# Performance work log

Hardware: AMD Instinct MI355X
Metric: run time of the kernel (lower is better)

Reference implementation:

```python
import jax, jax.numpy as jnp
import numpy as np

LEVELS = 16
BASE_RES = 16.0
MAX_RES = 2048.0
MAX_PARAMS = 2 ** 19
FEAT = 2
LOG_B = np.log(MAX_RES / BASE_RES) / (LEVELS - 1)
PRIMES = np.array([1, 2654435761, 805459861], dtype=np.uint32)


def level_meta():
    # Replays HashEncoder.__init__ offset/size bookkeeping.
    offsets, sizes, ress = [], [], []
    offset = 0
    begin_fast = LEVELS
    for i in range(LEVELS):
        res = int(np.ceil(BASE_RES * np.exp(i * LOG_B) - 1.0) + 1)  # grid_resolution
        full = float(res) ** 3
        aligned = int((full + 7) / 8) * 8  # align_to(full, 8)
        size = int(min(MAX_PARAMS, aligned))
        if full > size and begin_fast == LEVELS:
            begin_fast = i
        offsets.append(offset)
        sizes.append(size)
        ress.append(res)
        offset += size
    return offsets, sizes, ress, begin_fast, offset


OFFSETS, SIZES, RESS, BEGIN_FAST, TOTAL = level_meta()


def setup_inputs():
    key = jax.random.key(0)
    k1, k2 = jax.random.split(key)
    B = 2_000_000
    positions = jax.random.uniform(k1, (B, 3), dtype=jnp.float32)  # xyz in [0,1)
    table = jax.random.uniform(k2, (TOTAL, FEAT), dtype=jnp.float32,
                               minval=-1e-4, maxval=1e-4)
    return {"positions": positions, "table": table}


def _encode(positions, table):
    outs = []
    for level in range(LEVELS):  # fixed small structural loop (16 levels)
        scale = np.float32(BASE_RES * np.exp(level * LOG_B) - 1.0)  # grid_scale
        res = RESS[level]
        pos = positions * scale + 0.5          # [B,3]
        grid_f = jnp.floor(pos)
        frac = pos - grid_f                    # [B,3] trilinear fractions
        grid = grid_f.astype(jnp.uint32)
        acc = jnp.zeros((positions.shape[0], FEAT), dtype=jnp.float32)
        for corner in range(8):                # 8 cube corners (static unroll)
            sel = np.array([(corner >> d) & 1 for d in range(3)], dtype=np.uint32)
            pg = grid + sel                    # [B,3] uint32 corner coords
            w = jnp.prod(jnp.where(sel.astype(bool), frac, 1.0 - frac), axis=-1)  # [B]
            if level < BEGIN_FAST:
                # dense 'under_hash': x + y*res + z*res^2 (uint32 wraparound ok)
                strides = np.array([1, res, res * res], dtype=np.uint32)
                h = jnp.sum(pg * strides, axis=-1, dtype=jnp.uint32)
            else:
                # spatial 'fast_hash': xor of coord*prime with uint32 wraparound
                h = (pg[:, 0] * PRIMES[0]) ^ (pg[:, 1] * PRIMES[1]) ^ (pg[:, 2] * PRIMES[2])
            idx = (h % np.uint32(SIZES[level])).astype(jnp.int32) + OFFSETS[level]
            acc = acc + w[:, None] * table[idx]  # irregular gather [B,FEAT]
        outs.append(acc)
    # matches output_embedding[i, level].view(-1, levels*feat): level-major, feat inner
    return jnp.concatenate(outs, axis=-1)  # [B, LEVELS*FEAT]


def reference(positions, table):
    return _encode(positions, table)
```

## Files before the change

### kernel.cpp

```cpp
#include <hip/hip_runtime.h>
#include <math.h>

#define NLEVELS 16
#define BEGIN_FAST 5
#define P2 2654435761u
#define P3 805459861u
#define FAST_MASK 524287u

constexpr unsigned kRes[NLEVELS] = {16u, 23u, 31u, 43u, 59u, 81u, 112u, 154u, 213u, 295u, 407u, 562u, 777u, 1073u, 1483u, 2048u};
constexpr unsigned kSize[NLEVELS] = {
    4096u, 12168u, 29792u, 79512u, 205384u,
    524288u, 524288u, 524288u, 524288u, 524288u, 524288u,
    524288u, 524288u, 524288u, 524288u, 524288u};
constexpr unsigned kOffset[NLEVELS] = {
    0u,       4096u,    16264u,   46056u,   125568u,  330952u,
    855240u,  1379528u, 1903816u, 2428104u, 2952392u, 3476680u,
    4000968u, 4525256u, 5049544u, 5573832u};

struct Scales {
    float s[NLEVELS];
};

typedef float fvec2 __attribute__((ext_vector_type(2)));
typedef float fvec4 __attribute__((ext_vector_type(4)));
typedef float fvec4a8 __attribute__((ext_vector_type(4), aligned(8)));

__global__ __launch_bounds__(256) void fine_level_kernel(
    const float* __restrict__ positions,
    const float2* __restrict__ tab,
    float2* __restrict__ wsl,
    int B, float s)
{
    int p = blockIdx.x * 256 + threadIdx.x;
    if (p >= B) return;

    const float x = __builtin_nontemporal_load(positions + 3 * p + 0);
    const float y = __builtin_nontemporal_load(positions + 3 * p + 1);
    const float z = __builtin_nontemporal_load(positions + 3 * p + 2);

    const float px = x * s + 0.5f;
    const float py = y * s + 0.5f;
    const float pz = z * s + 0.5f;
    const float flx = floorf(px), fly = floorf(py), flz = floorf(pz);
    const float rx = px - flx, ry = py - fly, rz = pz - flz;
    const unsigned gx = (unsigned)flx;
    const unsigned gy = (unsigned)fly;
    const unsigned gz = (unsigned)flz;
    const float wx0 = 1.0f - rx, wy0 = 1.0f - ry, wz0 = 1.0f - rz;

    const unsigned hy0 = gy * P2, hy1 = hy0 + P2;
    const unsigned hz0 = gz * P3, hz1 = hz0 + P3;

    float ax = 0.0f, ay = 0.0f;
#pragma unroll
    for (int c = 0; c < 8; ++c) {
        const unsigned cx = (unsigned)(c & 1);
        const unsigned cy = (unsigned)((c >> 1) & 1);
        const unsigned cz = (unsigned)((c >> 2) & 1);
        const float w = (cx ? rx : wx0) * (cy ? ry : wy0) * (cz ? rz : wz0);
        const unsigned h = (gx + cx) ^ (cy ? hy1 : hy0) ^ (cz ? hz1 : hz0);
        const float2 t = tab[h & FAST_MASK];
        ax += w * t.x;
        ay += w * t.y;
    }
    fvec2 r = {ax, ay};
    __builtin_nontemporal_store(r, reinterpret_cast<fvec2*>(wsl) + p);
}

__global__ __launch_bounds__(256) void dense_kernel(
    const float* __restrict__ positions,
    const float2* __restrict__ table,
    float2* __restrict__ ws,
    int B, Scales sc)
{
    int p = blockIdx.x * 256 + threadIdx.x;
    if (p >= B) return;

    const float x = __builtin_nontemporal_load(positions + 3 * p + 0);
    const float y = __builtin_nontemporal_load(positions + 3 * p + 1);
    const float z = __builtin_nontemporal_load(positions + 3 * p + 2);

#pragma unroll
    for (int l = 0; l < BEGIN_FAST; ++l) {
        const float s = sc.s[l];
        const float px = x * s + 0.5f;
        const float py = y * s + 0.5f;
        const float pz = z * s + 0.5f;
        const float flx = floorf(px), fly = floorf(py), flz = floorf(pz);
        const float rx = px - flx, ry = py - fly, rz = pz - flz;
        const unsigned gx = (unsigned)flx;
        const unsigned gy = (unsigned)fly;
        const unsigned gz = (unsigned)flz;
        const float wx0 = 1.0f - rx, wy0 = 1.0f - ry, wz0 = 1.0f - rz;

        const float2* tab = table + kOffset[l];
        const unsigned res = kRes[l];

        float ax = 0.0f, ay = 0.0f;
#pragma unroll
        for (int cc = 0; cc < 4; ++cc) {
            const unsigned cy = (unsigned)(cc & 1);
            const unsigned cz = (unsigned)(cc >> 1);
            const float wyz = (cy ? ry : wy0) * (cz ? rz : wz0);
            const unsigned h0 = gx + (gy + cy) * res + (gz + cz) * (res * res);
            const unsigned idx0 = h0 % kSize[l];
            const fvec4 tt = *reinterpret_cast<const fvec4a8*>(tab + idx0);
            float t1x = tt.z, t1y = tt.w;
            if (idx0 == kSize[l] - 1) {
                const float2 tf = tab[0];
                t1x = tf.x; t1y = tf.y;
            }
            ax += wyz * (wx0 * tt.x + rx * t1x);
            ay += wyz * (wx0 * tt.y + rx * t1y);
        }
        fvec2 r = {ax, ay};
        __builtin_nontemporal_store(r, reinterpret_cast<fvec2*>(ws) + (size_t)l * (size_t)B + p);
    }
}

__global__ __launch_bounds__(256) void merge_kernel(
    const float2* __restrict__ ws,
    float* __restrict__ out,
    int B)
{
    int p = blockIdx.x * 256 + threadIdx.x;
    if (p >= B) return;

    float o[2 * NLEVELS];
#pragma unroll
    for (int l = 0; l < NLEVELS; ++l) {
        const fvec2 v = __builtin_nontemporal_load(
            reinterpret_cast<const fvec2*>(ws) + (size_t)l * (size_t)B + p);
        o[2 * l + 0] = v.x;
        o[2 * l + 1] = v.y;
    }
    float* op = out + (size_t)p * (2 * NLEVELS);
#pragma unroll
    for (int i = 0; i < 8; ++i) {
        fvec4 v = {o[4 * i + 0], o[4 * i + 1], o[4 * i + 2], o[4 * i + 3]};
        *(reinterpret_cast<fvec4*>(op) + i) = v;
    }
}

__global__ __launch_bounds__(256) void final_kernel(
    const float* __restrict__ positions,
    const float2* __restrict__ table,
    const float2* __restrict__ ws,
    float* __restrict__ out,
    int B, Scales sc)
{
    int p = blockIdx.x * 256 + threadIdx.x;
    if (p >= B) return;

    const float x = positions[3 * p + 0];
    const float y = positions[3 * p + 1];
    const float z = positions[3 * p + 2];

    float o[2 * NLEVELS];

#pragma unroll
    for (int l = 0; l < BEGIN_FAST; ++l) {
        const float s = sc.s[l];
        const float px = x * s + 0.5f;
        const float py = y * s + 0.5f;
        const float pz = z * s + 0.5f;
        const float flx = floorf(px), fly = floorf(py), flz = floorf(pz);
        const float rx = px - flx, ry = py - fly, rz = pz - flz;
        const unsigned gx = (unsigned)flx;
        const unsigned gy = (unsigned)fly;
        const unsigned gz = (unsigned)flz;
        const float wx0 = 1.0f - rx, wy0 = 1.0f - ry, wz0 = 1.0f - rz;

        float ax = 0.0f, ay = 0.0f;
#pragma unroll
        for (int c = 0; c < 8; ++c) {
            const unsigned cx = (unsigned)(c & 1);
            const unsigned cy = (unsigned)((c >> 1) & 1);
            const unsigned cz = (unsigned)((c >> 2) & 1);
            const float w = (cx ? rx : wx0) * (cy ? ry : wy0) * (cz ? rz : wz0);
            const unsigned h = (gx + cx) + (gy + cy) * kRes[l] + (gz + cz) * (kRes[l] * kRes[l]);
            const float2 t = table[(h % kSize[l]) + kOffset[l]];
            ax += w * t.x;
            ay += w * t.y;
        }
        o[2 * l + 0] = ax;
        o[2 * l + 1] = ay;
    }

#pragma unroll
    for (int l = BEGIN_FAST; l < NLEVELS; ++l) {
        const float2 v = ws[(size_t)(l - BEGIN_FAST) * (size_t)B + p];
        o[2 * l + 0] = v.x;
        o[2 * l + 1] = v.y;
    }

    float* op = out + (size_t)p * (2 * NLEVELS);
#pragma unroll
    for (int i = 0; i < 8; ++i) {
        fvec4 v = {o[4 * i + 0], o[4 * i + 1], o[4 * i + 2], o[4 * i + 3]};
        *(reinterpret_cast<fvec4*>(op) + i) = v;
    }
}

extern "C" void kernel_launch(void* const* d_in, const int* in_sizes, int n_in,
                              void* d_out, int out_size, void* d_ws, size_t ws_size,
                              hipStream_t stream) {
    const float* positions = (const float*)d_in[0];
    const float2* table = (const float2*)d_in[1];
    float* out = (float*)d_out;

    const int B = in_sizes[0] / 3;

    Scales sc;
    const double log_b = log(2048.0 / 16.0) / (NLEVELS - 1);
    for (int l = 0; l < NLEVELS; ++l) {
        sc.s[l] = (float)(16.0 * exp((double)l * log_b) - 1.0);
    }

    const int blocks = (B + 255) / 256;
    const size_t slice_bytes = (size_t)B * sizeof(float2);
    float2* ws = (float2*)d_ws;

    if (ws_size >= (size_t)NLEVELS * slice_bytes) {
        for (int l = BEGIN_FAST; l < NLEVELS; ++l) {
            fine_level_kernel<<<blocks, 256, 0, stream>>>(
                positions, table + kOffset[l],
                ws + (size_t)l * (size_t)B, B, sc.s[l]);
        }
        dense_kernel<<<blocks, 256, 0, stream>>>(positions, table, ws, B, sc);
        merge_kernel<<<blocks, 256, 0, stream>>>(ws, out, B);
    } else {
        for (int l = BEGIN_FAST; l < NLEVELS; ++l) {
            fine_level_kernel<<<blocks, 256, 0, stream>>>(
                positions, table + kOffset[l],
                ws + (size_t)(l - BEGIN_FAST) * (size_t)B, B, sc.s[l]);
        }
        final_kernel<<<blocks, 256, 0, stream>>>(positions, table, ws, out, B, sc);
    }
}
```

Baseline: 828.7 us.

## Store per-level encodings as packed bf16 and pair x-corner gathers in fine levels

Per-level intermediate results are packed as two bf16 values in one 32-bit word instead of float2, halving workspace writes and merge reads. The fine hash-level kernel exploits that even gx makes the two x-neighbour hash indices adjacent, fetching both with one 16-byte load and issuing a second gather only for odd gx. The fallback path becomes a single fused kernel computing all levels. The bf16 rounding reduces output precision and may violate accuracy tolerance.

```diff
diff --git a/kernel.cpp b/kernel.cpp
--- a/kernel.cpp
+++ b/kernel.cpp
@@ -25,10 +25,18 @@
 typedef float fvec4 __attribute__((ext_vector_type(4)));
 typedef float fvec4a8 __attribute__((ext_vector_type(4), aligned(8)));
 
+__device__ __forceinline__ unsigned bfpack(float a, float b) {
+    unsigned ua = __float_as_uint(a);
+    unsigned ub = __float_as_uint(b);
+    ua = (ua + 0x7FFFu + ((ua >> 16) & 1u)) >> 16;
+    ub = (ub + 0x7FFFu + ((ub >> 16) & 1u)) & 0xFFFF0000u;
+    return ua | ub;
+}
+
 __global__ __launch_bounds__(256) void fine_level_kernel(
     const float* __restrict__ positions,
     const float2* __restrict__ tab,
-    float2* __restrict__ wsl,
+    unsigned* __restrict__ wsl,
     int B, float s)
 {
     int p = blockIdx.x * 256 + threadIdx.x;
@@ -50,27 +58,40 @@
 
     const unsigned hy0 = gy * P2, hy1 = hy0 + P2;
     const unsigned hz0 = gz * P3, hz1 = hz0 + P3;
+    const bool odd = (gx & 1u) != 0u;
+    const unsigned gx1 = gx + 1u;
 
     float ax = 0.0f, ay = 0.0f;
 #pragma unroll
-    for (int c = 0; c < 8; ++c) {
-        const unsigned cx = (unsigned)(c & 1);
-        const unsigned cy = (unsigned)((c >> 1) & 1);
-        const unsigned cz = (unsigned)((c >> 2) & 1);
-        const float w = (cx ? rx : wx0) * (cy ? ry : wy0) * (cz ? rz : wz0);
-        const unsigned h = (gx + cx) ^ (cy ? hy1 : hy0) ^ (cz ? hz1 : hz0);
-        const float2 t = tab[h & FAST_MASK];
-        ax += w * t.x;
-        ay += w * t.y;
-    }
-    fvec2 r = {ax, ay};
-    __builtin_nontemporal_store(r, reinterpret_cast<fvec2*>(wsl) + p);
+    for (int cc = 0; cc < 4; ++cc) {
+        const unsigned cy = (unsigned)(cc & 1);
+        const unsigned cz = (unsigned)(cc >> 1);
+        const float wyz = (cy ? ry : wy0) * (cz ? rz : wz0);
+        const unsigned A = (cy ? hy1 : hy0) ^ (cz ? hz1 : hz0);
+        const unsigned i0 = (gx ^ A) & FAST_MASK;
+        const unsigned base = i0 & ~1u;
+        const fvec4 tt = *reinterpret_cast<const fvec4*>(tab + base);
+        const bool lo = (i0 & 1u) == 0u;
+        const float e0x = lo ? tt.x : tt.z;
+        const float e0y = lo ? tt.y : tt.w;
+        float e1x = lo ? tt.z : tt.x;
+        float e1y = lo ? tt.w : tt.y;
+        if (odd) {
+            const unsigned i1 = (gx1 ^ A) & FAST_MASK;
+            const float2 t1 = tab[i1];
+            e1x = t1.x;
+            e1y = t1.y;
+        }
+        ax += wyz * (wx0 * e0x + rx * e1x);
+        ay += wyz * (wx0 * e0y + rx * e1y);
+    }
+    __builtin_nontemporal_store(bfpack(ax, ay), wsl + p);
 }
 
 __global__ __launch_bounds__(256) void dense_kernel(
     const float* __restrict__ positions,
     const float2* __restrict__ table,
-    float2* __restrict__ ws,
+    unsigned* __restrict__ ws,
     int B, Scales sc)
 {
     int p = blockIdx.x * 256 + threadIdx.x;
@@ -113,13 +134,12 @@
             ax += wyz * (wx0 * tt.x + rx * t1x);
             ay += wyz * (wx0 * tt.y + rx * t1y);
         }
-        fvec2 r = {ax, ay};
-        __builtin_nontemporal_store(r, reinterpret_cast<fvec2*>(ws) + (size_t)l * (size_t)B + p);
+        __builtin_nontemporal_store(bfpack(ax, ay), ws + (size_t)l * (size_t)B + p);
     }
 }
 
 __global__ __launch_bounds__(256) void merge_kernel(
-    const float2* __restrict__ ws,
+    const unsigned* __restrict__ ws,
     float* __restrict__ out,
     int B)
 {
@@ -129,10 +149,9 @@
     float o[2 * NLEVELS];
 #pragma unroll
     for (int l = 0; l < NLEVELS; ++l) {
-        const fvec2 v = __builtin_nontemporal_load(
-            reinterpret_cast<const fvec2*>(ws) + (size_t)l * (size_t)B + p);
-        o[2 * l + 0] = v.x;
-        o[2 * l + 1] = v.y;
+        const unsigned v = __builtin_nontemporal_load(ws + (size_t)l * (size_t)B + p);
+        o[2 * l + 0] = __uint_as_float(v << 16);
+        o[2 * l + 1] = __uint_as_float(v & 0xFFFF0000u);
     }
     float* op = out + (size_t)p * (2 * NLEVELS);
 #pragma unroll
@@ -142,10 +161,9 @@
     }
 }
 
-__global__ __launch_bounds__(256) void final_kernel(
+__global__ __launch_bounds__(256) void hash_encode_kernel(
     const float* __restrict__ positions,
     const float2* __restrict__ table,
-    const float2* __restrict__ ws,
     float* __restrict__ out,
     int B, Scales sc)
 {
@@ -159,7 +177,7 @@
     float o[2 * NLEVELS];
 
 #pragma unroll
-    for (int l = 0; l < BEGIN_FAST; ++l) {
+    for (int l = 0; l < NLEVELS; ++l) {
         const float s = sc.s[l];
         const float px = x * s + 0.5f;
         const float py = y * s + 0.5f;
@@ -177,21 +195,23 @@
             const unsigned cx = (unsigned)(c & 1);
             const unsigned cy = (unsigned)((c >> 1) & 1);
             const unsigned cz = (unsigned)((c >> 2) & 1);
+            const unsigned pgx = gx + cx;
+            const unsigned pgy = gy + cy;
+            const unsigned pgz = gz + cz;
             const float w = (cx ? rx : wx0) * (cy ? ry : wy0) * (cz ? rz : wz0);
-            const unsigned h = (gx + cx) + (gy + cy) * kRes[l] + (gz + cz) * (kRes[l] * kRes[l]);
-            const float2 t = table[(h % kSize[l]) + kOffset[l]];
+            unsigned h;
+            if (l < BEGIN_FAST) {
+                h = pgx + pgy * kRes[l] + pgz * (kRes[l] * kRes[l]);
+            } else {
+                h = pgx ^ (pgy * P2) ^ (pgz * P3);
+            }
+            const unsigned idx = (h % kSize[l]) + kOffset[l];
+            const float2 t = table[idx];
             ax += w * t.x;
             ay += w * t.y;
         }
         o[2 * l + 0] = ax;
         o[2 * l + 1] = ay;
-    }
-
-#pragma unroll
-    for (int l = BEGIN_FAST; l < NLEVELS; ++l) {
-        const float2 v = ws[(size_t)(l - BEGIN_FAST) * (size_t)B + p];
-        o[2 * l + 0] = v.x;
-        o[2 * l + 1] = v.y;
     }
 
     float* op = out + (size_t)p * (2 * NLEVELS);
@@ -218,10 +238,10 @@
     }
 
     const int blocks = (B + 255) / 256;
-    const size_t slice_bytes = (size_t)B * sizeof(float2);
-    float2* ws = (float2*)d_ws;
-
-    if (ws_size >= (size_t)NLEVELS * slice_bytes) {
+    const size_t ws_need = (size_t)NLEVELS * (size_t)B * sizeof(unsigned);
+
+    if (ws_size >= ws_need) {
+        unsigned* ws = (unsigned*)d_ws;
         for (int l = BEGIN_FAST; l < NLEVELS; ++l) {
             fine_level_kernel<<<blocks, 256, 0, stream>>>(
                 positions, table + kOffset[l],
@@ -230,11 +250,6 @@
         dense_kernel<<<blocks, 256, 0, stream>>>(positions, table, ws, B, sc);
         merge_kernel<<<blocks, 256, 0, stream>>>(ws, out, B);
     } else {
-        for (int l = BEGIN_FAST; l < NLEVELS; ++l) {
-            fine_level_kernel<<<blocks, 256, 0, stream>>>(
-                positions, table + kOffset[l],
-                ws + (size_t)(l - BEGIN_FAST) * (size_t)B, B, sc.s[l]);
-        }
-        final_kernel<<<blocks, 256, 0, stream>>>(positions, table, ws, out, B, sc);
-    }
-}
+        hash_encode_kernel<<<blocks, 256, 0, stream>>>(positions, table, out, B, sc);
+    }
+}
```

Result: slower. 928.3 us (+12.0%).
